# Performance work log

Hardware: AMD Instinct MI355X
Metric: run time of the kernel (lower is better)

## Reference

```python
import jax, jax.numpy as jnp
import numpy as np

HIDDEN = 2048
NH = 32       # num query heads
NKV = 8       # num kv heads
D = 64        # head_dim = hidden // NH
BSX, BSY = 32, 32  # block sizes


def setup_inputs() -> dict:
    key = jax.random.key(0)
    ks = jax.random.split(key, 5)
    B, L = 2, 4096  # L = x_dim * y_dim
    w = lambda k, sh, fan: jax.random.normal(k, sh, jnp.float32) * (fan ** -0.5)
    return {
        "hidden_states": jax.random.normal(ks[0], (B, L, HIDDEN), jnp.float32),
        "Wq": w(ks[1], (HIDDEN, NH * D), HIDDEN),
        "Wk": w(ks[2], (HIDDEN, NKV * D), HIDDEN),
        "Wv": w(ks[3], (HIDDEN, NKV * D), HIDDEN),
        "Wo": w(ks[4], (NH * D, HIDDEN), NH * D),
        "x_dim": 64,
        "y_dim": 64,
    }


def _block_split(x, B, bnx, bny, h):
    # einops: 'b (bnx bsx bny bsy) (h d) -> (b bnx bny) (bsx bsy) h d'
    x = x.reshape(B, bnx, BSX, bny, BSY, h, D)
    x = x.transpose(0, 1, 3, 2, 4, 5, 6)  # b bnx bny bsx bsy h d
    return x.reshape(B * bnx * bny, BSX * BSY, h, D)


def reference(hidden_states, Wq, Wk, Wv, Wo, x_dim, y_dim):
    B, L, _ = hidden_states.shape
    bnx, bny = x_dim // BSX, y_dim // BSY
    q = _block_split(hidden_states @ Wq, B, bnx, bny, NH)   # [nb, T, NH, D]
    k = _block_split(hidden_states @ Wk, B, bnx, bny, NKV)  # [nb, T, NKV, D]
    v = _block_split(hidden_states @ Wv, B, bnx, bny, NKV)
    g = NH // NKV  # GQA groups: query head i attends kv head i // g
    k = jnp.repeat(k, g, axis=2)
    v = jnp.repeat(v, g, axis=2)
    scores = jnp.einsum('nqhd,nkhd->nhqk', q, k) * (D ** -0.5)
    p = jax.nn.softmax(scores, axis=-1)
    o = jnp.einsum('nhqk,nkhd->nqhd', p, v)  # [nb, T, NH, D]
    # Faithful to the torch code: plain reshape (does NOT invert the block rearrange)
    o = o.reshape(B, L, NH * D)
    return o @ Wo
```

## Files before the change

kernel.cpp:

```cpp
#include <hip/hip_runtime.h>

typedef __bf16 bf16_t;
typedef __bf16 bf16x8 __attribute__((ext_vector_type(8)));
typedef __bf16 bf16x4 __attribute__((ext_vector_type(4)));
typedef float f32x4 __attribute__((ext_vector_type(4)));
typedef float f32x16 __attribute__((ext_vector_type(16)));
typedef short s16x4 __attribute__((ext_vector_type(4)));
typedef short s16x8 __attribute__((ext_vector_type(8)));
typedef unsigned u32x2 __attribute__((ext_vector_type(2)));

#define MFMA16(A_, B_, C_) __builtin_amdgcn_mfma_f32_16x16x32_bf16((A_), (B_), (C_), 0, 0, 0)
#define MFMA32(A_, B_, C_) __builtin_amdgcn_mfma_f32_32x32x16_bf16((A_), (B_), (C_), 0, 0, 0)

#define QSC 0.18033688011112042f

#if __has_builtin(__builtin_amdgcn_exp2f)
#define EXP2F(x) __builtin_amdgcn_exp2f(x)
#else
#define EXP2F(x) exp2f(x)
#endif

__device__ __forceinline__ void gload_lds16(const bf16_t* g, bf16_t* l) {
  __builtin_amdgcn_global_load_lds(
      (const __attribute__((address_space(1))) void*)g,
      (__attribute__((address_space(3))) void*)l, 16, 0, 0);
}

__device__ __forceinline__ unsigned cvt_pk_bf16(float a, float b) {
  unsigned r;
  asm("v_cvt_pk_bf16_f32 %0, %1, %2" : "=v"(r) : "v"(a), "v"(b));
  return r;
}

__device__ __forceinline__ s16x4 tr_b16(const bf16_t* p) {
  s16x4 d;
  unsigned off = (unsigned)(size_t)(const __attribute__((address_space(3))) bf16_t*)p;
  asm volatile("ds_read_b64_tr_b16 %0, %1" : "=v"(d) : "v"(off));
  return d;
}

union B128 { s16x8 s; bf16x8 b; };

#define DSR(PTR, U)                                                           \
  do {                                                                        \
    unsigned _o = (unsigned)(size_t)                                          \
        (const __attribute__((address_space(3))) bf16_t*)(PTR);               \
    asm volatile("ds_read_b128 %0, %1" : "=v"((U).s) : "v"(_o));              \
  } while (0)

__device__ __forceinline__ void swap32(unsigned a, unsigned b, int hi,
                                       unsigned& ra, unsigned& rb) {
#if __has_builtin(__builtin_amdgcn_permlane32_swap)
  u32x2 r = __builtin_amdgcn_permlane32_swap(b, a, false, false);
  rb = r[0]; ra = r[1];
#else
  unsigned bx = (unsigned)__shfl_xor((int)b, 32);
  unsigned ax = (unsigned)__shfl_xor((int)a, 32);
  ra = hi ? a : bx;
  rb = hi ? ax : b;
#endif
}

__global__ __launch_bounds__(256) void k_convert(const float* __restrict__ in,
                                                 bf16_t* __restrict__ out, int n4) {
  int i = blockIdx.x * 256 + threadIdx.x;
  if (i >= n4) return;
  float4 v = ((const float4*)in)[i];
  bf16x4 o;
  o[0] = (__bf16)v.x; o[1] = (__bf16)v.y; o[2] = (__bf16)v.z; o[3] = (__bf16)v.w;
  *(bf16x4*)(out + (size_t)i * 4) = o;
}

__global__ __launch_bounds__(256) void k_transpose(const float* __restrict__ in,
                                                   bf16_t* __restrict__ out, int R, int C) {
  __shared__ float tile[64][65];
  int tx = threadIdx.x & 63;
  int ty = threadIdx.x >> 6;
  int bc = blockIdx.x * 64;
  int br = blockIdx.y * 64;
#pragma unroll
  for (int i = ty; i < 64; i += 4)
    tile[i][tx] = in[(size_t)(br + i) * C + bc + tx];
  __syncthreads();
#pragma unroll
  for (int i = ty; i < 64; i += 4)
    out[(size_t)(bc + i) * R + br + tx] = (bf16_t)tile[tx][i];
}

__device__ __forceinline__ int permrow(int r) {
  int b  = r >> 12;
  int l  = r & 4095;
  int ix = (l >> 11) & 1;
  int sx = (l >> 6) & 31;
  int iy = (l >> 5) & 1;
  int sy = l & 31;
  return (b << 12) + (ix << 11) + (iy << 10) + (sx << 5) + sy;
}

#define SBAR __builtin_amdgcn_sched_barrier(0)

#define LA(K_) (lds + (K_)*24576)
#define LB(K_) (lds + (K_)*24576 + 16384)

__global__ __launch_bounds__(512, 2) void k_gemmA(
    const bf16_t* __restrict__ A,
    const bf16_t* __restrict__ B0, const bf16_t* __restrict__ B1,
    const bf16_t* __restrict__ B2,
    bf16_t* __restrict__ Cq, bf16_t* __restrict__ Ck, bf16_t* __restrict__ Cv) {
  extern __shared__ bf16_t lds[];

  int bid = blockIdx.x;
  int s = bid >> 3;
  int tm = (bid & 7) * 4 + s / 24;
  int tn = s % 24;

  const bf16_t* Bp;
  int brow;
  if (tn < 16)      { Bp = B0; brow = tn << 7; }
  else if (tn < 20) { Bp = B1; brow = (tn - 16) << 7; }
  else              { Bp = B2; brow = (tn - 20) << 7; }

  int tid = threadIdx.x;
  int lane = tid & 63;
  int w = tid >> 6;
  int wm = w >> 1, wn = w & 1;
  int g16 = lane >> 4, cl = lane & 15;
  int swz8 = (cl & 7) << 3;
  int wofs = w << 9;

  int srow = tid >> 3;
  int lc = (((tid & 7) ^ (srow & 7)) << 3);
  const bf16_t* aB = A + (size_t)(tm * 256 + srow) * 2048 + lc;
  const bf16_t* bB = Bp + (size_t)(brow + srow) * 2048 + lc;

#define GA_STAGE_A(K_, T_)                                                     \
  _Pragma("unroll") for (int rr = 0; rr < 4; ++rr)                             \
    gload_lds16(aB + (size_t)(rr * 64) * 2048 + (T_)*64,                       \
                LA(K_) + rr * 4096 + wofs);

#define GA_STAGE_B(K_, T_)                                                     \
  _Pragma("unroll") for (int rr = 0; rr < 2; ++rr)                             \
    gload_lds16(bB + (size_t)(rr * 64) * 2048 + (T_)*64,                       \
                LB(K_) + rr * 4096 + wofs);

#define GA_RD_B(K_)                                                            \
  _Pragma("unroll") for (int ni = 0; ni < 4; ++ni) {                           \
    const bf16_t* Br = LB(K_) + (wn * 64 + ni * 16 + cl) * 64;                 \
    DSR(Br + ((g16 * 8) ^ swz8), bfr[ni][0]);                                  \
    DSR(Br + ((32 + g16 * 8) ^ swz8), bfr[ni][1]);                             \
  }

#define GA_RD_A(K_, MB_)                                                       \
  _Pragma("unroll") for (int m = 0; m < 2; ++m) {                              \
    const bf16_t* Ar = LA(K_) + (wm * 64 + ((MB_) + m) * 16 + cl) * 64;        \
    DSR(Ar + ((g16 * 8) ^ swz8), af[m][0]);                                    \
    DSR(Ar + ((32 + g16 * 8) ^ swz8), af[m][1]);                               \
  }

#define GA_MFMA(MB_)                                                           \
  _Pragma("unroll") for (int kk = 0; kk < 2; ++kk)                             \
    _Pragma("unroll") for (int m = 0; m < 2; ++m)                              \
      _Pragma("unroll") for (int ni = 0; ni < 4; ++ni)                         \
        acc[(MB_) + m][ni] =                                                   \
            MFMA16(af[m][kk].b, bfr[ni][kk].b, acc[(MB_) + m][ni]);

#define GA_MID                                                                 \
  __builtin_amdgcn_s_barrier();                                                \
  asm volatile("s_waitcnt lgkmcnt(0)" ::: "memory");                           \
  SBAR;                                                                        \
  __builtin_amdgcn_s_setprio(1);

#define GA_END                                                                 \
  SBAR;                                                                        \
  __builtin_amdgcn_s_setprio(0);                                               \
  __builtin_amdgcn_s_barrier();

  f32x4 acc[4][4];
#pragma unroll
  for (int i = 0; i < 4; ++i)
#pragma unroll
    for (int j = 0; j < 4; ++j) acc[i][j] = (f32x4)(0.0f);

  GA_STAGE_A(0, 0); GA_STAGE_B(0, 0);
  GA_STAGE_A(1, 1); GA_STAGE_B(1, 1);
  asm volatile("s_waitcnt vmcnt(6)" ::: "memory");
  __builtin_amdgcn_s_barrier();

  int k = 0;
  for (int t = 0; t < 32; ++t) {
    int k2 = k + 2; if (k2 >= 3) k2 -= 3;
    int t2 = t + 2; if (t2 > 31) t2 = 31;
    B128 af[2][2], bfr[4][2];
    GA_RD_B(k); GA_RD_A(k, 0);
    GA_STAGE_A(k2, t2);
    GA_MID; GA_MFMA(0); GA_END;
    GA_RD_A(k, 2);
    asm volatile("s_waitcnt vmcnt(4)" ::: "memory");
    GA_STAGE_B(k2, t2);
    GA_MID; GA_MFMA(2); GA_END;
    ++k; if (k == 3) k = 0;
  }

#pragma unroll
  for (int mi = 0; mi < 4; ++mi) {
#pragma unroll
    for (int rr = 0; rr < 4; ++rr) {
      int r = tm * 256 + wm * 64 + mi * 16 + g16 * 4 + rr;
      int rp = permrow(r);
#pragma unroll
      for (int ni = 0; ni < 4; ++ni) {
        int c = tn * 128 + wn * 64 + ni * 16 + cl;
        float v = acc[mi][ni][rr];
        if (c < 2048)      Cq[(size_t)rp * 2048 + c] = (bf16_t)(v * QSC);
        else if (c < 2560) Ck[(size_t)rp * 512 + (c - 2048)] = (bf16_t)v;
        else               Cv[(size_t)rp * 512 + (c - 2560)] = (bf16_t)v;
      }
    }
  }
}

#define LSLOT(B_, M_, H_) (lds + (((B_)*4 + (M_)*2 + (H_)) << 13))

#define STAGE_A(BUF, HF, T)                                                     \
  gload_lds16(aB + (size_t)((HF)*128) * 2048 + (T)*64, LSLOT(BUF, 0, HF) + wofs); \
  gload_lds16(aB + (size_t)((HF)*128 + 64) * 2048 + (T)*64,                     \
              LSLOT(BUF, 0, HF) + wofs + 4096);

#define STAGE_B(BUF, HF, T)                                                     \
  gload_lds16(bB + (size_t)((HF)*128) * 2048 + (T)*64, LSLOT(BUF, 1, HF) + wofs); \
  gload_lds16(bB + (size_t)((HF)*128 + 64) * 2048 + (T)*64,                     \
              LSLOT(BUF, 1, HF) + wofs + 4096);

#define LOAD_A(BUF, Q)                                                          \
  { const bf16_t* Ah = LSLOT(BUF, 0, wm) + ((Q)*32 + cl) * 64;                  \
    DSR(Ah + ((g16 * 8) ^ swz8), af[0][0]);                                     \
    DSR(Ah + ((32 + g16 * 8) ^ swz8), af[0][1]);                                \
    DSR(Ah + 1024 + ((g16 * 8) ^ swz8), af[1][0]);                              \
    DSR(Ah + 1024 + ((32 + g16 * 8) ^ swz8), af[1][1]); }

#define LOAD_B(BUF)                                                             \
  { const bf16_t* Bh = LSLOT(BUF, 1, wn >> 1);                                  \
    _Pragma("unroll") for (int ni = 0; ni < 4; ++ni) {                          \
      const bf16_t* Br = Bh + ((wn & 1) * 64 + ni * 16 + cl) * 64;              \
      DSR(Br + ((g16 * 8) ^ swz8), bfr[ni][0]);                                 \
      DSR(Br + ((32 + g16 * 8) ^ swz8), bfr[ni][1]); } }

#define MFMA_QUAD(Q)                                                            \
  _Pragma("unroll") for (int kk = 0; kk < 2; ++kk)                              \
    _Pragma("unroll") for (int ni = 0; ni < 4; ++ni) {                          \
      acc[2*(Q)][ni]   = MFMA16(af[0][kk].b, bfr[ni][kk].b, acc[2*(Q)][ni]);    \
      acc[2*(Q)+1][ni] = MFMA16(af[1][kk].b, bfr[ni][kk].b, acc[2*(Q)+1][ni]); }

#define PH_MID(VM4)                                                             \
  if (VM4) asm volatile("s_waitcnt vmcnt(4)" ::: "memory");                     \
  __builtin_amdgcn_s_barrier();                                                 \
  asm volatile("s_waitcnt lgkmcnt(0)" ::: "memory");                            \
  SBAR;                                                                         \
  __builtin_amdgcn_s_setprio(1);

#define PH_END                                                                  \
  SBAR;                                                                         \
  __builtin_amdgcn_s_setprio(0);                                                \
  __builtin_amdgcn_s_barrier();

__global__ __launch_bounds__(512, 2) void k_gemmB(
    const bf16_t* __restrict__ A, const bf16_t* __restrict__ B0,
    float* __restrict__ Cf) {
  extern __shared__ bf16_t lds[];

  int bid = blockIdx.x;
  int s = bid >> 3;
  int tm = (bid & 7) * 4 + (s >> 3);
  int tn = s & 7;
  const bf16_t* Bp = B0;
  int brow = tn << 8;

  int tid = threadIdx.x;
  int lane = tid & 63;
  int w = tid >> 6;
  int wm = w >> 2, wn = w & 3;
  int g16 = lane >> 4, cl = lane & 15;
  int swz8 = (cl & 7) << 3;
  int wofs = w << 9;

  int srow = tid >> 3;
  int lc = (((tid & 7) ^ (srow & 7)) << 3);
  const bf16_t* aB = A + (size_t)(tm * 256 + srow) * 2048 + lc;
  const bf16_t* bB = Bp + (size_t)(brow + srow) * 2048 + lc;

  f32x4 acc[8][4];
#pragma unroll
  for (int i = 0; i < 8; ++i)
#pragma unroll
    for (int j = 0; j < 4; ++j) acc[i][j] = (f32x4)(0.0f);

  STAGE_A(0, 0, 0); STAGE_A(0, 1, 0);
  STAGE_B(0, 0, 0); STAGE_B(0, 1, 0);
  STAGE_B(1, 0, 1); STAGE_B(1, 1, 1);
  asm volatile("s_waitcnt vmcnt(4)" ::: "memory");
  __builtin_amdgcn_s_barrier();

  for (int it2 = 0; it2 < 16; ++it2) {
    int t1 = 2 * it2 + 1;
    int tf = 2 * it2 + 2; if (tf > 31) tf = 31;
    int tg = 2 * it2 + 3; if (tg > 31) tg = 31;
    B128 af[2][2], bfr[4][2];
    STAGE_A(1, 0, t1);
    LOAD_B(0); LOAD_A(0, 0);
    PH_MID(0); MFMA_QUAD(0); PH_END;
    STAGE_A(1, 1, t1);
    LOAD_A(0, 1);
    PH_MID(0); MFMA_QUAD(1); PH_END;
    STAGE_B(0, 0, tf);
    LOAD_A(0, 2);
    PH_MID(0); MFMA_QUAD(2); PH_END;
    STAGE_B(0, 1, tf);
    LOAD_A(0, 3);
    PH_MID(1); MFMA_QUAD(3); PH_END;
    STAGE_A(0, 0, tf);
    LOAD_B(1); LOAD_A(1, 0);
    PH_MID(0); MFMA_QUAD(0); PH_END;
    STAGE_A(0, 1, tf);
    LOAD_A(1, 1);
    PH_MID(0); MFMA_QUAD(1); PH_END;
    STAGE_B(1, 0, tg);
    LOAD_A(1, 2);
    PH_MID(0); MFMA_QUAD(2); PH_END;
    STAGE_B(1, 1, tg);
    LOAD_A(1, 3);
    PH_MID(1); MFMA_QUAD(3); PH_END;
  }

#pragma unroll
  for (int mi = 0; mi < 8; ++mi) {
#pragma unroll
    for (int rr = 0; rr < 4; ++rr) {
      int r = tm * 256 + wm * 128 + mi * 16 + g16 * 4 + rr;
#pragma unroll
      for (int ni = 0; ni < 4; ++ni) {
        int c = tn * 256 + wn * 64 + ni * 16 + cl;
        Cf[(size_t)r * 2048 + c] = acc[mi][ni][rr];
      }
    }
  }
}

__global__ __launch_bounds__(256, 2) void k_attn(
    const bf16_t* __restrict__ Qp, const bf16_t* __restrict__ Kp,
    const bf16_t* __restrict__ Vp, bf16_t* __restrict__ O) {
  int bid = blockIdx.x;
  int qc = bid & 7;
  int h  = (bid >> 3) & 31;
  int n  = bid >> 8;
  int kvh = h >> 2;

  __shared__ bf16_t buf[2][8192];

  int tid = threadIdx.x, lane = tid & 63, w = tid >> 6;
  int l31 = lane & 31, hi = lane >> 5;
  int qrow_blk = n * 1024 + qc * 128;
  bf16_t* base = &buf[0][0];

#pragma unroll
  for (int r = 0; r < 4; ++r) {
    int ql = r * 32 + (tid >> 3);
    int cs = (tid & 7) << 4;
    int lc = (cs ^ ((ql & 7) << 4)) >> 1;
    gload_lds16(Qp + (size_t)(qrow_blk + ql) * 2048 + h * 64 + lc,
                base + r * 2048 + w * 512);
  }
  __syncthreads();
  bf16x8 qf[4];
  {
    int q = w * 32 + l31;
    const bf16_t* qrow = base + q * 64;
    int sw = (q & 7) << 4;
#pragma unroll
    for (int c = 0; c < 4; ++c)
      qf[c] = *(const bf16x8*)(qrow + (((c * 32 + hi * 16) ^ sw) >> 1));
  }
  __syncthreads();

  f32x16 oacc0 = (f32x16)(0.0f), oacc1 = (f32x16)(0.0f);
  float m_run = -1e30f, l_run = 0.0f;

  auto stageKV = [&](int t) {
    bf16_t* bp = &buf[t & 1][0];
    int kvb = n * 1024 + t * 64;
#pragma unroll
    for (int r = 0; r < 2; ++r) {
      int kv = r * 32 + (tid >> 3);
      int cs = (tid & 7) << 4;
      int lc = (cs ^ ((kv & 7) << 4)) >> 1;
      gload_lds16(Kp + (size_t)(kvb + kv) * 512 + kvh * 64 + lc,
                  bp + r * 2048 + w * 512);
    }
#pragma unroll
    for (int r = 0; r < 2; ++r) {
      int slot = r * 256 + tid;
      int sub = slot >> 3;
      int kb = sub >> 2, db = sub & 3;
      int j = (slot >> 1) & 3, hf = slot & 1;
      gload_lds16(Vp + (size_t)(kvb + kb * 4 + j) * 512 + kvh * 64 + db * 16 + hf * 8,
                  bp + 4096 + r * 2048 + w * 512);
    }
  };

  stageKV(0);
  for (int t = 0; t < 16; ++t) {
    __syncthreads();
    if (t < 15) stageKV(t + 1);
    const bf16_t* bp = &buf[t & 1][0];
    const bf16_t* Vs = bp + 4096;

#pragma unroll
    for (int s = 0; s < 2; ++s) {
      f32x16 st = (f32x16)(0.0f);
      {
        int kv = s * 32 + l31;
        const bf16_t* krow = bp + kv * 64;
        int sw = (kv & 7) << 4;
#pragma unroll
        for (int c = 0; c < 4; ++c) {
          bf16x8 kf = *(const bf16x8*)(krow + (((c * 32 + hi * 16) ^ sw) >> 1));
          st = MFMA32(kf, qf[c], st);
        }
      }
      float p0 = fmaxf(fmaxf(st[0], st[1]), st[2]);
      float p1 = fmaxf(fmaxf(st[3], st[4]), st[5]);
      float p2 = fmaxf(fmaxf(st[6], st[7]), st[8]);
      float p3 = fmaxf(fmaxf(st[9], st[10]), st[11]);
      float p4 = fmaxf(fmaxf(st[12], st[13]), st[14]);
      float pmax = fmaxf(fmaxf(fmaxf(p0, p1), p2),
                         fmaxf(fmaxf(p3, p4), st[15]));
      pmax = fmaxf(pmax, __shfl_xor(pmax, 32));
      if (!__all(pmax <= m_run + 11.0f)) {
        float mnew = fmaxf(m_run, pmax);
        float resc = EXP2F(m_run - mnew);
        l_run *= resc;
#pragma unroll
        for (int e = 0; e < 16; ++e) { oacc0[e] *= resc; oacc1[e] *= resc; }
        m_run = mnew;
      }
      float rs = 0.0f;
      unsigned pw[8];
#pragma unroll
      for (int u = 0; u < 8; ++u) {
        float q0 = EXP2F(st[2 * u] - m_run);
        float q1 = EXP2F(st[2 * u + 1] - m_run);
        rs += q0 + q1;
        pw[u] = cvt_pk_bf16(q0, q1);
      }
      rs += __shfl_xor(rs, 32);
      l_run += rs;

#pragma unroll
      for (int c = 0; c < 2; ++c) {
        unsigned w2, w0, w3, w1;
        swap32(pw[c * 4 + 2], pw[c * 4 + 0], hi, w2, w0);
        swap32(pw[c * 4 + 3], pw[c * 4 + 1], hi, w3, w1);
        union { unsigned u[4]; bf16x8 v; } pa;
        pa.u[0] = w0; pa.u[1] = w1; pa.u[2] = w2; pa.u[3] = w3;
        int kb0 = s * 8 + c * 4 + hi * 2;
        int dbl = l31 >> 4;
        int cc8 = (l31 & 15) * 4;
        const bf16_t* p00 = Vs + (kb0 * 4 + dbl) * 64 + cc8;
        const bf16_t* p01 = Vs + ((kb0 + 1) * 4 + dbl) * 64 + cc8;
        const bf16_t* p10 = Vs + (kb0 * 4 + 2 + dbl) * 64 + cc8;
        const bf16_t* p11 = Vs + ((kb0 + 1) * 4 + 2 + dbl) * 64 + cc8;
        s16x4 t00 = tr_b16(p00), t01 = tr_b16(p01);
        s16x4 t10 = tr_b16(p10), t11 = tr_b16(p11);
        asm volatile("s_waitcnt lgkmcnt(0)" ::: "memory");
        __builtin_amdgcn_sched_barrier(0);
        union { s16x4 s4[2]; bf16x8 v; } vf0, vf1;
        vf0.s4[0] = t00; vf0.s4[1] = t01;
        vf1.s4[0] = t10; vf1.s4[1] = t11;
        oacc0 = MFMA32(pa.v, vf0.v, oacc0);
        oacc1 = MFMA32(pa.v, vf1.v, oacc1);
      }
    }
  }

  float linv = 1.0f / l_run;
#pragma unroll
  for (int r = 0; r < 16; ++r) {
    int qrw = (r & 3) + 8 * (r >> 2) + 4 * hi;
    float li = __shfl(linv, qrw);
    size_t orow = (size_t)(qrow_blk + w * 32 + qrw) * 2048 + h * 64 + l31;
    O[orow]      = (bf16_t)(oacc0[r] * li);
    O[orow + 32] = (bf16_t)(oacc1[r] * li);
  }
}

extern "C" void kernel_launch(void* const* d_in, const int* in_sizes, int n_in,
                              void* d_out, int out_size, void* d_ws, size_t ws_size,
                              hipStream_t stream) {
  const float* X  = (const float*)d_in[0];
  const float* Wq = (const float*)d_in[1];
  const float* Wk = (const float*)d_in[2];
  const float* Wv = (const float*)d_in[3];
  const float* Wo = (const float*)d_in[4];
  float* out = (float*)d_out;

  char* ws = (char*)d_ws;
  const size_t MB = 1024 * 1024;
  bf16_t* Xb  = (bf16_t*)(ws + 0);
  bf16_t* WqT = (bf16_t*)(ws + 32 * MB);
  bf16_t* WkT = (bf16_t*)(ws + 40 * MB);
  bf16_t* WvT = (bf16_t*)(ws + 42 * MB);
  bf16_t* WoT = (bf16_t*)(ws + 44 * MB);
  bf16_t* Qp  = (bf16_t*)(ws + 52 * MB);
  bf16_t* Kp  = (bf16_t*)(ws + 84 * MB);
  bf16_t* Vp  = (bf16_t*)(ws + 92 * MB);
  bf16_t* Ob  = (bf16_t*)(ws + 100 * MB);

  hipFuncSetAttribute(reinterpret_cast<const void*>(&k_gemmA),
                      hipFuncAttributeMaxDynamicSharedMemorySize, 147456);
  hipFuncSetAttribute(reinterpret_cast<const void*>(&k_gemmB),
                      hipFuncAttributeMaxDynamicSharedMemorySize, 131072);

  k_convert<<<16384, 256, 0, stream>>>(X, Xb, 4194304);
  k_transpose<<<dim3(32, 32), 256, 0, stream>>>(Wq, WqT, 2048, 2048);
  k_transpose<<<dim3(8, 32), 256, 0, stream>>>(Wk, WkT, 2048, 512);
  k_transpose<<<dim3(8, 32), 256, 0, stream>>>(Wv, WvT, 2048, 512);
  k_transpose<<<dim3(32, 32), 256, 0, stream>>>(Wo, WoT, 2048, 2048);

  k_gemmA<<<768, 512, 147456, stream>>>(Xb, WqT, WkT, WvT, Qp, Kp, Vp);
  k_attn<<<2048, 256, 0, stream>>>(Qp, Kp, Vp, Ob);
  k_gemmB<<<256, 512, 131072, stream>>>(Ob, WoT, out);
}
```

Baseline: 324.6 us.

## Collapse GEMM main loop to one barrier per K-tile with full A read

Restructures the QKV projection GEMM main loop. It now waits on outstanding loads and syncs once per K-tile, reads all A and B fragments from LDS, issues both next-tile global-to-LDS stages, and runs all MFMAs in a single prioritized block. This replaces the previous two-phase ping-pong that had four barriers per iteration. The aim is lower barrier and synchronization overhead, at the cost of more fragment registers and less interleaving of loads with MFMA.

```diff
diff --git a/kernel.cpp b/kernel.cpp
--- a/kernel.cpp
+++ b/kernel.cpp
@@ -150,30 +150,18 @@
     DSR(Br + ((32 + g16 * 8) ^ swz8), bfr[ni][1]);                             \
   }
 
-#define GA_RD_A(K_, MB_)                                                       \
-  _Pragma("unroll") for (int m = 0; m < 2; ++m) {                              \
-    const bf16_t* Ar = LA(K_) + (wm * 64 + ((MB_) + m) * 16 + cl) * 64;        \
+#define GA_RD_A4(K_)                                                           \
+  _Pragma("unroll") for (int m = 0; m < 4; ++m) {                              \
+    const bf16_t* Ar = LA(K_) + (wm * 64 + m * 16 + cl) * 64;                  \
     DSR(Ar + ((g16 * 8) ^ swz8), af[m][0]);                                    \
     DSR(Ar + ((32 + g16 * 8) ^ swz8), af[m][1]);                               \
   }
 
-#define GA_MFMA(MB_)                                                           \
+#define GA_MFMA_ALL                                                            \
   _Pragma("unroll") for (int kk = 0; kk < 2; ++kk)                             \
-    _Pragma("unroll") for (int m = 0; m < 2; ++m)                              \
+    _Pragma("unroll") for (int m = 0; m < 4; ++m)                              \
       _Pragma("unroll") for (int ni = 0; ni < 4; ++ni)                         \
-        acc[(MB_) + m][ni] =                                                   \
-            MFMA16(af[m][kk].b, bfr[ni][kk].b, acc[(MB_) + m][ni]);
-
-#define GA_MID                                                                 \
-  __builtin_amdgcn_s_barrier();                                                \
-  asm volatile("s_waitcnt lgkmcnt(0)" ::: "memory");                           \
-  SBAR;                                                                        \
-  __builtin_amdgcn_s_setprio(1);
-
-#define GA_END                                                                 \
-  SBAR;                                                                        \
-  __builtin_amdgcn_s_setprio(0);                                               \
-  __builtin_amdgcn_s_barrier();
+        acc[m][ni] = MFMA16(af[m][kk].b, bfr[ni][kk].b, acc[m][ni]);
 
   f32x4 acc[4][4];
 #pragma unroll
@@ -183,21 +171,21 @@
 
   GA_STAGE_A(0, 0); GA_STAGE_B(0, 0);
   GA_STAGE_A(1, 1); GA_STAGE_B(1, 1);
-  asm volatile("s_waitcnt vmcnt(6)" ::: "memory");
-  __builtin_amdgcn_s_barrier();
 
   int k = 0;
   for (int t = 0; t < 32; ++t) {
     int k2 = k + 2; if (k2 >= 3) k2 -= 3;
     int t2 = t + 2; if (t2 > 31) t2 = 31;
-    B128 af[2][2], bfr[4][2];
-    GA_RD_B(k); GA_RD_A(k, 0);
-    GA_STAGE_A(k2, t2);
-    GA_MID; GA_MFMA(0); GA_END;
-    GA_RD_A(k, 2);
-    asm volatile("s_waitcnt vmcnt(4)" ::: "memory");
-    GA_STAGE_B(k2, t2);
-    GA_MID; GA_MFMA(2); GA_END;
+    B128 af[4][2], bfr[4][2];
+    asm volatile("s_waitcnt vmcnt(6)" ::: "memory");
+    __builtin_amdgcn_s_barrier();
+    GA_RD_B(k); GA_RD_A4(k);
+    GA_STAGE_A(k2, t2); GA_STAGE_B(k2, t2);
+    asm volatile("s_waitcnt lgkmcnt(0)" ::: "memory");
+    SBAR;
+    __builtin_amdgcn_s_setprio(1);
+    GA_MFMA_ALL;
+    __builtin_amdgcn_s_setprio(0);
     ++k; if (k == 3) k = 0;
   }
 
```

Result: no change. 326.1 us (+0.5%).
